# Performance work log

Measured on AMD Instinct MI355X. Metric: run time of the kernel, lower is better.

The kernel has to match this reference:

```python
import jax, jax.numpy as jnp
import numpy as np

B, T, N, F, H, HEADS = 4, 10, 2048, 64, 128, 4
D = H // HEADS
E = 65536
NTOT = B * N


def setup_inputs() -> dict:
    key = jax.random.key(0)
    ks = jax.random.split(key, 16)
    s = 0.05
    return {
        "x": jax.random.normal(ks[0], (B, T, N, F), jnp.float32),
        "W": jax.random.normal(ks[1], (F, H), jnp.float32) * s,
        "att_src": jax.random.normal(ks[2], (HEADS, D), jnp.float32) * s,
        "att_dst": jax.random.normal(ks[3], (HEADS, D), jnp.float32) * s,
        "gat_bias": jnp.zeros((H,), jnp.float32),
        "W_ih0": jax.random.normal(ks[4], (4 * H, H), jnp.float32) * s,
        "W_hh0": jax.random.normal(ks[5], (4 * H, H), jnp.float32) * s,
        "b_ih0": jnp.zeros((4 * H,), jnp.float32),
        "b_hh0": jnp.zeros((4 * H,), jnp.float32),
        "W_ih1": jax.random.normal(ks[6], (4 * H, H), jnp.float32) * s,
        "W_hh1": jax.random.normal(ks[7], (4 * H, H), jnp.float32) * s,
        "b_ih1": jnp.zeros((4 * H,), jnp.float32),
        "b_hh1": jnp.zeros((4 * H,), jnp.float32),
        "ln_gamma": jnp.ones((H,), jnp.float32),
        "ln_beta": jnp.zeros((H,), jnp.float32),
        "edge_index": jax.random.randint(ks[8], (2, E), 0, NTOT, dtype=jnp.int32),
    }


def reference(x, W, att_src, att_dst, gat_bias,
              W_ih0, W_hh0, b_ih0, b_hh0,
              W_ih1, W_hh1, b_ih1, b_hh1,
              ln_gamma, ln_beta, edge_index):
    # ---- GAT spatial encoding, vectorized over all T timesteps ----
    loops = jnp.arange(NTOT, dtype=edge_index.dtype)  # PyG GATConv adds self-loops
    src = jnp.concatenate([edge_index[0], loops])
    dst = jnp.concatenate([edge_index[1], loops])

    x_flat = x.transpose(1, 0, 2, 3).reshape(T, NTOT, F)          # [T, B*N, F]
    h = (x_flat @ W).reshape(T, NTOT, HEADS, D)                    # per-head projections
    a_src = jnp.einsum('tnhd,hd->tnh', h, att_src)                 # [T, NTOT, HEADS]
    a_dst = jnp.einsum('tnhd,hd->tnh', h, att_dst)
    e = jax.nn.leaky_relu(a_src[:, src] + a_dst[:, dst], 0.2)      # [T, Ef, HEADS]

    def seg_softmax(e_t):
        m = jax.ops.segment_max(e_t, dst, num_segments=NTOT)
        ex = jnp.exp(e_t - m[dst])
        den = jax.ops.segment_sum(ex, dst, num_segments=NTOT)
        return ex / den[dst]

    alpha = jax.vmap(seg_softmax)(e)                               # edge softmax per target
    msg = alpha[..., None] * h[:, src]                             # [T, Ef, HEADS, D]
    agg = jax.vmap(lambda m: jax.ops.segment_sum(m, dst, num_segments=NTOT))(msg)
    spatial = jax.nn.relu(agg.reshape(T, NTOT, H) + gat_bias)      # concat heads + bias + relu

    # ---- 2-layer LSTM over time (batched over all B*N node sequences) ----
    def step(carry, xt):
        h0, c0, h1, c1 = carry
        g0 = xt @ W_ih0.T + h0 @ W_hh0.T + (b_ih0 + b_hh0)
        i, f, g, o = jnp.split(g0, 4, axis=-1)
        c0 = jax.nn.sigmoid(f) * c0 + jax.nn.sigmoid(i) * jnp.tanh(g)
        h0 = jax.nn.sigmoid(o) * jnp.tanh(c0)
        g1 = h0 @ W_ih1.T + h1 @ W_hh1.T + (b_ih1 + b_hh1)
        i, f, g, o = jnp.split(g1, 4, axis=-1)
        c1 = jax.nn.sigmoid(f) * c1 + jax.nn.sigmoid(i) * jnp.tanh(g)
        h1 = jax.nn.sigmoid(o) * jnp.tanh(c1)
        return (h0, c0, h1, c1), None

    z = jnp.zeros((NTOT, H), spatial.dtype)
    (_, _, h1, _), _ = jax.lax.scan(step, (z, z, z, z), spatial)
    ctx = h1.reshape(B, N, H)

    # ---- LayerNorm ----
    mu = ctx.mean(-1, keepdims=True)
    var = ctx.var(-1, keepdims=True)
    return (ctx - mu) / jnp.sqrt(var + 1e-5) * ln_gamma + ln_beta
```

## Files before the change

### kernel.cpp

```cpp
#include <hip/hip_runtime.h>

#define T_ 10
#define B_ 4
#define N_ 2048
#define NTOT 8192
#define F_ 64
#define H_ 128
#define NHEADS 4
#define D_ 32
#define E_ 65536
#define EF 73728
#define HPAD 136

typedef __bf16 bf16x8 __attribute__((ext_vector_type(8)));
typedef float f32x4 __attribute__((ext_vector_type(4)));
typedef unsigned short u16;

__device__ __forceinline__ float bf2f(u16 u){
  union { unsigned int i; float f; } v; v.i = ((unsigned int)u) << 16; return v.f;
}
__device__ __forceinline__ u16 f2bf(float f){
  union { float f; unsigned int i; } v; v.f = f;
  return (u16)((v.i + 0x7FFFu + ((v.i >> 16) & 1u)) >> 16);
}
__device__ __forceinline__ float rcpf(float x){ return __builtin_amdgcn_rcpf(x); }
__device__ __forceinline__ float sigf(float x){ return rcpf(1.f + __expf(-x)); }
__device__ __forceinline__ float tanhfast(float x){ return 1.f - 2.f * rcpf(__expf(2.f * x) + 1.f); }
__device__ __forceinline__ float lrelu(float x){ return x > 0.f ? x : 0.2f * x; }

__global__ __launch_bounds__(256) void k_init(int* __restrict__ cnt){
  int i = blockIdx.x * 256 + threadIdx.x;
  if(i < NTOT) cnt[i] = 0;
}

__global__ __launch_bounds__(256) void k_count(const int* __restrict__ ei, int* __restrict__ cnt){
  int e = blockIdx.x * 256 + threadIdx.x;
  if(e < E_) atomicAdd(&cnt[ei[E_ + e]], 1);
}

__global__ __launch_bounds__(1024) void k_scan(const int* __restrict__ cnt,
                                               int* __restrict__ rowst,
                                               int* __restrict__ cursor){
  __shared__ int lds[1024];
  const int t = threadIdx.x;
  int loc[8];
  int s = 0;
  #pragma unroll
  for(int i = 0; i < 8; i++){ loc[i] = s; s += cnt[t * 8 + i]; }
  lds[t] = s;
  __syncthreads();
  for(int off = 1; off < 1024; off <<= 1){
    int v = lds[t];
    int a = (t >= off) ? lds[t - off] : 0;
    __syncthreads();
    lds[t] = v + a;
    __syncthreads();
  }
  const int base = (t > 0) ? lds[t - 1] : 0;
  #pragma unroll
  for(int i = 0; i < 8; i++){
    rowst[t * 8 + i] = base + loc[i];
    cursor[t * 8 + i] = 0;
  }
  if(t == 1023) rowst[NTOT] = lds[1023];
}

__global__ __launch_bounds__(256) void k_fill(const int* __restrict__ ei,
                                              const int* __restrict__ rowst,
                                              int* __restrict__ cursor,
                                              int* __restrict__ csr,
                                              int* __restrict__ csr_dst){
  int e = blockIdx.x * 256 + threadIdx.x;
  if(e < E_){
    int d = ei[E_ + e];
    int pos = atomicAdd(&cursor[d], 1);
    csr[rowst[d] + pos] = ei[e];
    csr_dst[rowst[d] + pos] = d;
  }
}

__global__ __launch_bounds__(256) void k_wconv(const float* __restrict__ s0, u16* __restrict__ d0,
                                               const float* __restrict__ s1, u16* __restrict__ d1,
                                               const float* __restrict__ s2, u16* __restrict__ d2,
                                               const float* __restrict__ s3, u16* __restrict__ d3,
                                               const float* __restrict__ W, u16* __restrict__ Wt){
  int i = blockIdx.x * 256 + threadIdx.x;
  if(blockIdx.y == 4){
    if(i < H_ * F_){
      int nn = i >> 6, f = i & 63;
      Wt[i] = f2bf(W[f * H_ + nn]);
    }
    return;
  }
  const float* src = blockIdx.y == 0 ? s0 : blockIdx.y == 1 ? s1 : blockIdx.y == 2 ? s2 : s3;
  u16* dst = blockIdx.y == 0 ? d0 : blockIdx.y == 1 ? d1 : blockIdx.y == 2 ? d2 : d3;
  if(i < 512 * 128){
    int p = i >> 7, k = i & 127;
    int w = p >> 6, g = (p >> 4) & 3, l = p & 15;
    int row = g * 128 + w * 16 + l;
    dst[i] = f2bf(src[row * 128 + k]);
  }
}

__global__ __launch_bounds__(256) void k_projm(const float* __restrict__ x,
    const u16* __restrict__ Wt, const float* __restrict__ att_s, const float* __restrict__ att_d,
    u16* __restrict__ hbuf, float* __restrict__ asrc, float* __restrict__ adst){
  const int tid  = threadIdx.x;
  const int wave = tid >> 6;
  const int lane = tid & 63;
  const int l15  = lane & 15;
  const int quad = lane >> 4;
  const int r0   = blockIdx.x * 64 + wave * 16;
  const int row  = r0 + l15;
  const int t = row >> 13, nt = row & 8191;
  const int b = nt >> 11, n = nt & 2047;
  const float* xrow = x + (((size_t)b * T_ + t) * N_ + n) * F_;

  bf16x8 a[2];
  #pragma unroll
  for(int ks = 0; ks < 2; ks++){
    const float4 f0 = *(const float4*)(xrow + ks * 32 + quad * 8);
    const float4 f1 = *(const float4*)(xrow + ks * 32 + quad * 8 + 4);
    bf16x8 av;
    av[0] = (__bf16)f0.x; av[1] = (__bf16)f0.y; av[2] = (__bf16)f0.z; av[3] = (__bf16)f0.w;
    av[4] = (__bf16)f1.x; av[5] = (__bf16)f1.y; av[6] = (__bf16)f1.z; av[7] = (__bf16)f1.w;
    a[ks] = av;
  }

  f32x4 acc[8];
  #pragma unroll
  for(int c = 0; c < 8; c++){ f32x4 z = {0.f,0.f,0.f,0.f}; acc[c] = z; }
  #pragma unroll
  for(int c = 0; c < 8; c++){
    #pragma unroll
    for(int ks = 0; ks < 2; ks++){
      const bf16x8 bv = *(const bf16x8*)(Wt + (c * 16 + l15) * F_ + ks * 32 + quad * 8);
      acc[c] = __builtin_amdgcn_mfma_f32_16x16x32_bf16(a[ks], bv, acc[c], 0, 0, 0);
    }
  }

  float ps[4][4], pd[4][4];
  #pragma unroll
  for(int r = 0; r < 4; r++)
    #pragma unroll
    for(int h = 0; h < 4; h++){ ps[r][h] = 0.f; pd[r][h] = 0.f; }

  #pragma unroll
  for(int c = 0; c < 8; c++){
    const int col = c * 16 + l15;
    const float asv = att_s[col];
    const float adv = att_d[col];
    const int head = c >> 1;
    #pragma unroll
    for(int r = 0; r < 4; r++){
      const float v = acc[c][r];
      hbuf[(size_t)(r0 + quad * 4 + r) * H_ + col] = f2bf(v);
      ps[r][head] += v * asv;
      pd[r][head] += v * adv;
    }
  }
  #pragma unroll
  for(int m = 8; m >= 1; m >>= 1){
    #pragma unroll
    for(int r = 0; r < 4; r++)
      #pragma unroll
      for(int h = 0; h < 4; h++){
        ps[r][h] += __shfl_xor(ps[r][h], m);
        pd[r][h] += __shfl_xor(pd[r][h], m);
      }
  }
  if(l15 == 0){
    #pragma unroll
    for(int r = 0; r < 4; r++){
      const int rw = r0 + quad * 4 + r;
      #pragma unroll
      for(int h = 0; h < 4; h++){
        asrc[(size_t)rw * NHEADS + h] = ps[r][h];
        adst[(size_t)rw * NHEADS + h] = pd[r][h];
      }
    }
  }
}

__global__ __launch_bounds__(256) void k_mden(const float* __restrict__ asrc,
    const float* __restrict__ adst, const int* __restrict__ rowst, const int* __restrict__ csr,
    float* __restrict__ m_, float* __restrict__ den_){
  const int gid = blockIdx.x * 256 + threadIdx.x;
  const int head = gid & 3;
  const int node = (gid >> 2) & 8191;
  const int t = gid >> 15;
  const int rbase = t * NTOT;
  const float ad = adst[(size_t)(rbase + node) * NHEADS + head];
  float m = lrelu(asrc[(size_t)(rbase + node) * NHEADS + head] + ad);
  float den = 1.f;
  const int rs = rowst[node], re = rowst[node + 1];
  for(int i = rs; i < re; i++){
    const int s = csr[i];
    const float ev = lrelu(asrc[(size_t)(rbase + s) * NHEADS + head] + ad);
    const float nm = fmaxf(m, ev);
    den = den * __expf(m - nm) + __expf(ev - nm);
    m = nm;
  }
  m_[gid] = m;
  den_[gid] = den;
}

__global__ __launch_bounds__(256) void k_alpha(const float* __restrict__ asrc,
    const float* __restrict__ adst, const int* __restrict__ csr, const int* __restrict__ csr_dst,
    const float* __restrict__ m_, const float* __restrict__ den_, float* __restrict__ alphaC){
  const int p = blockIdx.x * 256 + threadIdx.x;
  const int t = blockIdx.y;
  const int rbase = t * NTOT;
  int s, d;
  if(p < E_){ s = csr[p]; d = csr_dst[p]; } else { s = d = p - E_; }
  const float4 as4 = *(const float4*)&asrc[(size_t)(rbase + s) * NHEADS];
  const float4 ad4 = *(const float4*)&adst[(size_t)(rbase + d) * NHEADS];
  const float4 m4  = *(const float4*)&m_[(size_t)(rbase + d) * NHEADS];
  const float4 dn4 = *(const float4*)&den_[(size_t)(rbase + d) * NHEADS];
  float4 o;
  o.x = __expf(lrelu(as4.x + ad4.x) - m4.x) * rcpf(dn4.x);
  o.y = __expf(lrelu(as4.y + ad4.y) - m4.y) * rcpf(dn4.y);
  o.z = __expf(lrelu(as4.z + ad4.z) - m4.z) * rcpf(dn4.z);
  o.w = __expf(lrelu(as4.w + ad4.w) - m4.w) * rcpf(dn4.w);
  *(float4*)&alphaC[((size_t)t * EF + p) * NHEADS] = o;
}

__global__ __launch_bounds__(256) void k_agg(const u16* __restrict__ hbuf,
    const float* __restrict__ alphaC, const int* __restrict__ rowst, const int* __restrict__ csr,
    const float* __restrict__ gbias, u16* __restrict__ spat){
  const int tid = threadIdx.x;
  const int wave = tid >> 6;
  const int lane = tid & 63;
  const int task = blockIdx.x * 4 + wave;
  const int node = task & 8191;
  const int t = task >> 13;
  const int rbase = t * NTOT;
  const int d0 = lane, d1 = lane + 64;

  const float4 aself = *(const float4*)&alphaC[((size_t)t * EF + E_ + node) * NHEADS];
  float acc0 = (lane < 32 ? aself.x : aself.y) * bf2f(hbuf[(size_t)(rbase + node) * H_ + d0]);
  float acc1 = (lane < 32 ? aself.z : aself.w) * bf2f(hbuf[(size_t)(rbase + node) * H_ + d1]);
  const int rs = rowst[node], re = rowst[node + 1];
  for(int i = rs; i < re; i++){
    const int s = csr[i];
    const float4 av = *(const float4*)&alphaC[((size_t)t * EF + i) * NHEADS];
    const float a0 = lane < 32 ? av.x : av.y;
    const float a1 = lane < 32 ? av.z : av.w;
    acc0 += a0 * bf2f(hbuf[(size_t)(rbase + s) * H_ + d0]);
    acc1 += a1 * bf2f(hbuf[(size_t)(rbase + s) * H_ + d1]);
  }
  const float v0 = acc0 + gbias[d0];
  const float v1 = acc1 + gbias[d1];
  spat[(size_t)(rbase + node) * H_ + d0] = f2bf(v0 > 0.f ? v0 : 0.f);
  spat[(size_t)(rbase + node) * H_ + d1] = f2bf(v1 > 0.f ? v1 : 0.f);
}

__global__ __launch_bounds__(512) void k_lstm(
    const u16* __restrict__ spat,
    const u16* __restrict__ Wp_ih0, const u16* __restrict__ Wp_hh0,
    const float* __restrict__ bih0, const float* __restrict__ bhh0,
    const u16* __restrict__ Wp_ih1, const u16* __restrict__ Wp_hh1,
    const float* __restrict__ bih1, const float* __restrict__ bhh1,
    const float* __restrict__ lng, const float* __restrict__ lnb,
    float* __restrict__ out)
{
  __shared__ __align__(16) u16 xin[32 * HPAD];
  __shared__ __align__(16) u16 h0s[2][32 * HPAD];
  __shared__ __align__(16) u16 h1s[2][32 * HPAD];
  __shared__ __align__(16) float hfin[32 * 129];
  __shared__ float cst_l[16][512];
  __shared__ float bias_l[8][512];

  const int tid  = threadIdx.x;
  const int wave = tid >> 6;
  const int lane = tid & 63;
  const int l15  = lane & 15;
  const int quad = lane >> 4;
  const int n0   = blockIdx.x * 32;
  const int dim  = wave * 16 + l15;

  for(int i = tid; i < 2 * 32 * HPAD; i += 512){
    ((u16*)h0s)[i] = 0; ((u16*)h1s)[i] = 0;
  }
  {
    const u16* src = spat + (size_t)n0 * H_;
    const int r = tid >> 4, c = tid & 15;
    *(uint4*)(xin + r * HPAD + c * 8) = *(const uint4*)(src + r * 128 + c * 8);
  }
  #pragma unroll
  for(int i = 0; i < 16; i++) cst_l[i][tid] = 0.f;
  #pragma unroll
  for(int g = 0; g < 4; g++){
    bias_l[g][tid]     = bih0[g * 128 + dim] + bhh0[g * 128 + dim];
    bias_l[4 + g][tid] = bih1[g * 128 + dim] + bhh1[g * 128 + dim];
  }
  __syncthreads();

  const size_t fbase = (size_t)(wave * 64 + l15) * 128 + quad * 8;

#define LOADB(BK, MATB, KS, NTO)                                          \
    BK[0] = *(const bf16x8*)((MATB) + (NTO) * 2048 + (KS) * 32);          \
    BK[1] = *(const bf16x8*)((MATB) + ((NTO) + 1) * 2048 + (KS) * 32);

#define LOADA(AP, KS)                                                     \
    a0 = *(const bf16x8*)((AP) + l15 * HPAD + (KS) * 32 + quad * 8);      \
    a1 = *(const bf16x8*)((AP) + (16 + l15) * HPAD + (KS) * 32 + quad * 8);

#define MM(BK, NTO)                                                                             \
    acc[0][NTO]       = __builtin_amdgcn_mfma_f32_16x16x32_bf16(a0, BK[0], acc[0][NTO], 0, 0, 0);       \
    acc[1][NTO]       = __builtin_amdgcn_mfma_f32_16x16x32_bf16(a1, BK[0], acc[1][NTO], 0, 0, 0);       \
    acc[0][(NTO) + 1] = __builtin_amdgcn_mfma_f32_16x16x32_bf16(a0, BK[1], acc[0][(NTO) + 1], 0, 0, 0); \
    acc[1][(NTO) + 1] = __builtin_amdgcn_mfma_f32_16x16x32_bf16(a1, BK[1], acc[1][(NTO) + 1], 0, 0, 0); \
    __builtin_amdgcn_sched_barrier(0);

  #pragma unroll 1
  for(int t = 0; t < T_; t++){
    const int rp = t & 1, wp = rp ^ 1;
    #pragma unroll
    for(int layer = 0; layer < 2; layer++){
      const u16* Wih = layer ? Wp_ih1 : Wp_ih0;
      const u16* Whh = layer ? Wp_hh1 : Wp_hh0;
      const u16* xp  = layer ? h0s[wp] : xin;
      const u16* hp  = layer ? h1s[rp] : h0s[rp];

      f32x4 acc[2][4];
      #pragma unroll
      for(int nt = 0; nt < 4; nt++){
        const float bv = bias_l[layer * 4 + nt][tid];
        f32x4 b4 = {bv, bv, bv, bv};
        acc[0][nt] = b4; acc[1][nt] = b4;
      }

      const u16* WihB = Wih + fbase;
      const u16* WhhB = Whh + fbase;
      bf16x8 bA[2], bB[2], bC[2];
      bf16x8 a0, a1;

      LOADB(bA, WihB, 0, 0)  LOADB(bB, WihB, 0, 2)  LOADA(xp, 0)
      LOADB(bC, WihB, 1, 0)  MM(bA, 0)
      LOADB(bA, WihB, 1, 2)  MM(bB, 2)
      LOADA(xp, 1)  LOADB(bB, WihB, 2, 0)  MM(bC, 0)
      LOADB(bC, WihB, 2, 2)  MM(bA, 2)
      LOADA(xp, 2)  LOADB(bA, WihB, 3, 0)  MM(bB, 0)
      LOADB(bB, WihB, 3, 2)  MM(bC, 2)
      LOADA(xp, 3)  LOADB(bC, WhhB, 0, 0)  MM(bA, 0)
      LOADB(bA, WhhB, 0, 2)  MM(bB, 2)
      LOADA(hp, 0)  LOADB(bB, WhhB, 1, 0)  MM(bC, 0)
      LOADB(bC, WhhB, 1, 2)  MM(bA, 2)
      LOADA(hp, 1)  LOADB(bA, WhhB, 2, 0)  MM(bB, 0)
      LOADB(bB, WhhB, 2, 2)  MM(bC, 2)
      LOADA(hp, 2)  LOADB(bC, WhhB, 3, 0)  MM(bA, 0)
      LOADB(bA, WhhB, 3, 2)  MM(bB, 2)
      LOADA(hp, 3)  MM(bC, 0)
      MM(bA, 2)

      u16* hcur = layer ? h1s[wp] : h0s[wp];
      #pragma unroll
      for(int mt = 0; mt < 2; mt++){
        #pragma unroll
        for(int r = 0; r < 4; r++){
          const int node = mt * 16 + quad * 4 + r;
          const float gi = acc[mt][0][r];
          const float gf = acc[mt][1][r];
          const float gg = acc[mt][2][r];
          const float go = acc[mt][3][r];
          const int ci = layer * 8 + mt * 4 + r;
          const float c = sigf(gf) * cst_l[ci][tid] + sigf(gi) * tanhfast(gg);
          cst_l[ci][tid] = c;
          const float hv = sigf(go) * tanhfast(c);
          hcur[node * HPAD + dim] = f2bf(hv);
          if(layer == 1 && t == T_ - 1)
            hfin[node * 129 + dim] = hv;
        }
      }
      if(layer == 1 && t < T_ - 1){
        const u16* src = spat + (size_t)((t + 1) * NTOT + n0) * H_;
        const int r = tid >> 4, c = tid & 15;
        *(uint4*)(xin + r * HPAD + c * 8) = *(const uint4*)(src + r * 128 + c * 8);
      }
      __syncthreads();
    }
  }
#undef MM
#undef LOADA
#undef LOADB

  {
    const int node = tid >> 4;
    const int c0 = (tid & 15) * 8;
    float v[8];
    #pragma unroll
    for(int j = 0; j < 8; j++) v[j] = hfin[node * 129 + c0 + j];
    float s = 0.f;
    #pragma unroll
    for(int j = 0; j < 8; j++) s += v[j];
    #pragma unroll
    for(int m = 8; m >= 1; m >>= 1) s += __shfl_xor(s, m);
    const float mu = s * (1.f / H_);
    float q = 0.f;
    #pragma unroll
    for(int j = 0; j < 8; j++){ const float d = v[j] - mu; q += d * d; }
    #pragma unroll
    for(int m = 8; m >= 1; m >>= 1) q += __shfl_xor(q, m);
    const float rstd = rsqrtf(q * (1.f / H_) + 1e-5f);
    #pragma unroll
    for(int j = 0; j < 8; j++)
      out[(size_t)(n0 + node) * H_ + c0 + j] = (v[j] - mu) * rstd * lng[c0 + j] + lnb[c0 + j];
  }
}

extern "C" void kernel_launch(void* const* d_in, const int* in_sizes, int n_in,
                              void* d_out, int out_size, void* d_ws, size_t ws_size,
                              hipStream_t stream) {
  (void)in_sizes; (void)n_in; (void)out_size; (void)ws_size;
  const float* x     = (const float*)d_in[0];
  const float* W     = (const float*)d_in[1];
  const float* att_s = (const float*)d_in[2];
  const float* att_d = (const float*)d_in[3];
  const float* gbias = (const float*)d_in[4];
  const float* Wih0  = (const float*)d_in[5];
  const float* Whh0  = (const float*)d_in[6];
  const float* bih0  = (const float*)d_in[7];
  const float* bhh0  = (const float*)d_in[8];
  const float* Wih1  = (const float*)d_in[9];
  const float* Whh1  = (const float*)d_in[10];
  const float* bih1  = (const float*)d_in[11];
  const float* bhh1  = (const float*)d_in[12];
  const float* lng   = (const float*)d_in[13];
  const float* lnb   = (const float*)d_in[14];
  const int*   ei    = (const int*)d_in[15];
  float* out = (float*)d_out;

  char* p = (char*)d_ws;
  auto carve = [&](size_t bytes) -> void* {
    void* r = (void*)p;
    p += (bytes + 255) & ~(size_t)255;
    return r;
  };
  u16* Wp_ih0 = (u16*)carve(512 * 128 * 2);
  u16* Wp_hh0 = (u16*)carve(512 * 128 * 2);
  u16* Wp_ih1 = (u16*)carve(512 * 128 * 2);
  u16* Wp_hh1 = (u16*)carve(512 * 128 * 2);
  u16* Wt     = (u16*)carve(H_ * F_ * 2);
  u16*   hbuf   = (u16*)carve((size_t)T_ * NTOT * H_ * 2);
  float* asrc   = (float*)carve((size_t)T_ * NTOT * NHEADS * 4);
  float* adst   = (float*)carve((size_t)T_ * NTOT * NHEADS * 4);
  float* m_     = (float*)carve((size_t)T_ * NTOT * NHEADS * 4);
  float* den_   = (float*)carve((size_t)T_ * NTOT * NHEADS * 4);
  float* alphaC = (float*)carve((size_t)T_ * EF * NHEADS * 4);
  u16*   spat   = (u16*)carve((size_t)T_ * NTOT * H_ * 2);
  int*   cnt    = (int*)carve(NTOT * 4);
  int*   curs   = (int*)carve(NTOT * 4);
  int*   rowst  = (int*)carve((NTOT + 1) * 4);
  int*   csr    = (int*)carve((size_t)E_ * 4);
  int*   csrd   = (int*)carve((size_t)E_ * 4);

  hipLaunchKernelGGL(k_init,  dim3(32),        dim3(256),  0, stream, cnt);
  hipLaunchKernelGGL(k_count, dim3(256),       dim3(256),  0, stream, ei, cnt);
  hipLaunchKernelGGL(k_scan,  dim3(1),         dim3(1024), 0, stream, cnt, rowst, curs);
  hipLaunchKernelGGL(k_fill,  dim3(256),       dim3(256),  0, stream, ei, rowst, curs, csr, csrd);
  hipLaunchKernelGGL(k_wconv, dim3(256, 5),    dim3(256),  0, stream,
                     Wih0, Wp_ih0, Whh0, Wp_hh0, Wih1, Wp_ih1, Whh1, Wp_hh1, W, Wt);
  hipLaunchKernelGGL(k_projm, dim3(1280),      dim3(256),  0, stream, x, Wt, att_s, att_d, hbuf, asrc, adst);
  hipLaunchKernelGGL(k_mden,  dim3(1280),      dim3(256),  0, stream, asrc, adst, rowst, csr, m_, den_);
  hipLaunchKernelGGL(k_alpha, dim3(288, 10),   dim3(256),  0, stream, asrc, adst, csr, csrd, m_, den_, alphaC);
  hipLaunchKernelGGL(k_agg,   dim3(20480),     dim3(256),  0, stream, hbuf, alphaC, rowst, csr, gbias, spat);
  hipLaunchKernelGGL(k_lstm,  dim3(256),       dim3(512),  0, stream, spat,
                     Wp_ih0, Wp_hh0, bih0, bhh0, Wp_ih1, Wp_hh1, bih1, bhh1, lng, lnb, out);
}
```

Measured before the change: 338.3 us.

## Fuse GAT softmax max/denominator, alpha, and aggregation into one kernel

Replaces the separate k_mden, k_alpha and k_agg kernels with a single per-node wave kernel. Each wave computes the online softmax max and denominator over its incoming edges with a lane-parallel pass and a shuffle reduction, then recomputes the edge weights on the fly while aggregating neighbour features. This removes two launches and the global round trips through the m, den and alpha buffers. In exchange, every lane recomputes exp and leaky-relu for each edge in the aggregation loop.

```diff
diff --git a/kernel.cpp b/kernel.cpp
--- a/kernel.cpp
+++ b/kernel.cpp
@@ -182,51 +182,9 @@
   }
 }
 
-__global__ __launch_bounds__(256) void k_mden(const float* __restrict__ asrc,
-    const float* __restrict__ adst, const int* __restrict__ rowst, const int* __restrict__ csr,
-    float* __restrict__ m_, float* __restrict__ den_){
-  const int gid = blockIdx.x * 256 + threadIdx.x;
-  const int head = gid & 3;
-  const int node = (gid >> 2) & 8191;
-  const int t = gid >> 15;
-  const int rbase = t * NTOT;
-  const float ad = adst[(size_t)(rbase + node) * NHEADS + head];
-  float m = lrelu(asrc[(size_t)(rbase + node) * NHEADS + head] + ad);
-  float den = 1.f;
-  const int rs = rowst[node], re = rowst[node + 1];
-  for(int i = rs; i < re; i++){
-    const int s = csr[i];
-    const float ev = lrelu(asrc[(size_t)(rbase + s) * NHEADS + head] + ad);
-    const float nm = fmaxf(m, ev);
-    den = den * __expf(m - nm) + __expf(ev - nm);
-    m = nm;
-  }
-  m_[gid] = m;
-  den_[gid] = den;
-}
-
-__global__ __launch_bounds__(256) void k_alpha(const float* __restrict__ asrc,
-    const float* __restrict__ adst, const int* __restrict__ csr, const int* __restrict__ csr_dst,
-    const float* __restrict__ m_, const float* __restrict__ den_, float* __restrict__ alphaC){
-  const int p = blockIdx.x * 256 + threadIdx.x;
-  const int t = blockIdx.y;
-  const int rbase = t * NTOT;
-  int s, d;
-  if(p < E_){ s = csr[p]; d = csr_dst[p]; } else { s = d = p - E_; }
-  const float4 as4 = *(const float4*)&asrc[(size_t)(rbase + s) * NHEADS];
-  const float4 ad4 = *(const float4*)&adst[(size_t)(rbase + d) * NHEADS];
-  const float4 m4  = *(const float4*)&m_[(size_t)(rbase + d) * NHEADS];
-  const float4 dn4 = *(const float4*)&den_[(size_t)(rbase + d) * NHEADS];
-  float4 o;
-  o.x = __expf(lrelu(as4.x + ad4.x) - m4.x) * rcpf(dn4.x);
-  o.y = __expf(lrelu(as4.y + ad4.y) - m4.y) * rcpf(dn4.y);
-  o.z = __expf(lrelu(as4.z + ad4.z) - m4.z) * rcpf(dn4.z);
-  o.w = __expf(lrelu(as4.w + ad4.w) - m4.w) * rcpf(dn4.w);
-  *(float4*)&alphaC[((size_t)t * EF + p) * NHEADS] = o;
-}
-
-__global__ __launch_bounds__(256) void k_agg(const u16* __restrict__ hbuf,
-    const float* __restrict__ alphaC, const int* __restrict__ rowst, const int* __restrict__ csr,
+__global__ __launch_bounds__(256) void k_gat(const u16* __restrict__ hbuf,
+    const float* __restrict__ asrc, const float* __restrict__ adst,
+    const int* __restrict__ rowst, const int* __restrict__ csr,
     const float* __restrict__ gbias, u16* __restrict__ spat){
   const int tid = threadIdx.x;
   const int wave = tid >> 6;
@@ -235,24 +193,62 @@
   const int node = task & 8191;
   const int t = task >> 13;
   const int rbase = t * NTOT;
-  const int d0 = lane, d1 = lane + 64;
-
-  const float4 aself = *(const float4*)&alphaC[((size_t)t * EF + E_ + node) * NHEADS];
-  float acc0 = (lane < 32 ? aself.x : aself.y) * bf2f(hbuf[(size_t)(rbase + node) * H_ + d0]);
-  float acc1 = (lane < 32 ? aself.z : aself.w) * bf2f(hbuf[(size_t)(rbase + node) * H_ + d1]);
   const int rs = rowst[node], re = rowst[node + 1];
+
+  const float4 ad4  = *(const float4*)&adst[(size_t)(rbase + node) * NHEADS];
+  const float4 ass4 = *(const float4*)&asrc[(size_t)(rbase + node) * NHEADS];
+  const float es0 = lrelu(ass4.x + ad4.x), es1 = lrelu(ass4.y + ad4.y);
+  const float es2 = lrelu(ass4.z + ad4.z), es3 = lrelu(ass4.w + ad4.w);
+
+  float m0, m1, m2, m3, d0, d1, d2, d3;
+  if(lane == 0){ m0 = es0; m1 = es1; m2 = es2; m3 = es3; d0 = d1 = d2 = d3 = 1.f; }
+  else { m0 = m1 = m2 = m3 = -1e30f; d0 = d1 = d2 = d3 = 0.f; }
+  for(int i = rs + lane; i < re; i += 64){
+    const int s = csr[i];
+    const float4 as4 = *(const float4*)&asrc[(size_t)(rbase + s) * NHEADS];
+    const float e0 = lrelu(as4.x + ad4.x), e1 = lrelu(as4.y + ad4.y);
+    const float e2 = lrelu(as4.z + ad4.z), e3 = lrelu(as4.w + ad4.w);
+    float nm;
+    nm = fmaxf(m0, e0); d0 = d0 * __expf(m0 - nm) + __expf(e0 - nm); m0 = nm;
+    nm = fmaxf(m1, e1); d1 = d1 * __expf(m1 - nm) + __expf(e1 - nm); m1 = nm;
+    nm = fmaxf(m2, e2); d2 = d2 * __expf(m2 - nm) + __expf(e2 - nm); m2 = nm;
+    nm = fmaxf(m3, e3); d3 = d3 * __expf(m3 - nm) + __expf(e3 - nm); m3 = nm;
+  }
+  #pragma unroll
+  for(int msk = 32; msk >= 1; msk >>= 1){
+    float mo, dn, nm;
+    mo = __shfl_xor(m0, msk); dn = __shfl_xor(d0, msk);
+    nm = fmaxf(m0, mo); d0 = d0 * __expf(m0 - nm) + dn * __expf(mo - nm); m0 = nm;
+    mo = __shfl_xor(m1, msk); dn = __shfl_xor(d1, msk);
+    nm = fmaxf(m1, mo); d1 = d1 * __expf(m1 - nm) + dn * __expf(mo - nm); m1 = nm;
+    mo = __shfl_xor(m2, msk); dn = __shfl_xor(d2, msk);
+    nm = fmaxf(m2, mo); d2 = d2 * __expf(m2 - nm) + dn * __expf(mo - nm); m2 = nm;
+    mo = __shfl_xor(m3, msk); dn = __shfl_xor(d3, msk);
+    nm = fmaxf(m3, mo); d3 = d3 * __expf(m3 - nm) + dn * __expf(mo - nm); m3 = nm;
+  }
+
+  const int dlo = lane, dhi = lane + 64;
+  const float mA  = lane < 32 ? m0 : m1;
+  const float mB  = lane < 32 ? m2 : m3;
+  const float rdA = rcpf(lane < 32 ? d0 : d1);
+  const float rdB = rcpf(lane < 32 ? d2 : d3);
+  const float esA = lane < 32 ? es0 : es1;
+  const float esB = lane < 32 ? es2 : es3;
+
+  float acc0 = __expf(esA - mA) * rdA * bf2f(hbuf[(size_t)(rbase + node) * H_ + dlo]);
+  float acc1 = __expf(esB - mB) * rdB * bf2f(hbuf[(size_t)(rbase + node) * H_ + dhi]);
   for(int i = rs; i < re; i++){
     const int s = csr[i];
-    const float4 av = *(const float4*)&alphaC[((size_t)t * EF + i) * NHEADS];
-    const float a0 = lane < 32 ? av.x : av.y;
-    const float a1 = lane < 32 ? av.z : av.w;
-    acc0 += a0 * bf2f(hbuf[(size_t)(rbase + s) * H_ + d0]);
-    acc1 += a1 * bf2f(hbuf[(size_t)(rbase + s) * H_ + d1]);
-  }
-  const float v0 = acc0 + gbias[d0];
-  const float v1 = acc1 + gbias[d1];
-  spat[(size_t)(rbase + node) * H_ + d0] = f2bf(v0 > 0.f ? v0 : 0.f);
-  spat[(size_t)(rbase + node) * H_ + d1] = f2bf(v1 > 0.f ? v1 : 0.f);
+    const float4 as4 = *(const float4*)&asrc[(size_t)(rbase + s) * NHEADS];
+    const float eA = lane < 32 ? lrelu(as4.x + ad4.x) : lrelu(as4.y + ad4.y);
+    const float eB = lane < 32 ? lrelu(as4.z + ad4.z) : lrelu(as4.w + ad4.w);
+    acc0 += __expf(eA - mA) * rdA * bf2f(hbuf[(size_t)(rbase + s) * H_ + dlo]);
+    acc1 += __expf(eB - mB) * rdB * bf2f(hbuf[(size_t)(rbase + s) * H_ + dhi]);
+  }
+  const float v0 = acc0 + gbias[dlo];
+  const float v1 = acc1 + gbias[dhi];
+  spat[(size_t)(rbase + node) * H_ + dlo] = f2bf(v0 > 0.f ? v0 : 0.f);
+  spat[(size_t)(rbase + node) * H_ + dhi] = f2bf(v1 > 0.f ? v1 : 0.f);
 }
 
 __global__ __launch_bounds__(512) void k_lstm(
@@ -445,9 +441,6 @@
   u16*   hbuf   = (u16*)carve((size_t)T_ * NTOT * H_ * 2);
   float* asrc   = (float*)carve((size_t)T_ * NTOT * NHEADS * 4);
   float* adst   = (float*)carve((size_t)T_ * NTOT * NHEADS * 4);
-  float* m_     = (float*)carve((size_t)T_ * NTOT * NHEADS * 4);
-  float* den_   = (float*)carve((size_t)T_ * NTOT * NHEADS * 4);
-  float* alphaC = (float*)carve((size_t)T_ * EF * NHEADS * 4);
   u16*   spat   = (u16*)carve((size_t)T_ * NTOT * H_ * 2);
   int*   cnt    = (int*)carve(NTOT * 4);
   int*   curs   = (int*)carve(NTOT * 4);
@@ -462,9 +455,7 @@
   hipLaunchKernelGGL(k_wconv, dim3(256, 5),    dim3(256),  0, stream,
                      Wih0, Wp_ih0, Whh0, Wp_hh0, Wih1, Wp_ih1, Whh1, Wp_hh1, W, Wt);
   hipLaunchKernelGGL(k_projm, dim3(1280),      dim3(256),  0, stream, x, Wt, att_s, att_d, hbuf, asrc, adst);
-  hipLaunchKernelGGL(k_mden,  dim3(1280),      dim3(256),  0, stream, asrc, adst, rowst, csr, m_, den_);
-  hipLaunchKernelGGL(k_alpha, dim3(288, 10),   dim3(256),  0, stream, asrc, adst, csr, csrd, m_, den_, alphaC);
-  hipLaunchKernelGGL(k_agg,   dim3(20480),     dim3(256),  0, stream, hbuf, alphaC, rowst, csr, gbias, spat);
+  hipLaunchKernelGGL(k_gat,   dim3(20480),     dim3(256),  0, stream, hbuf, asrc, adst, rowst, csr, gbias, spat);
   hipLaunchKernelGGL(k_lstm,  dim3(256),       dim3(512),  0, stream, spat,
                      Wp_ih0, Wp_hh0, bih0, bhh0, Wp_ih1, Wp_hh1, bih1, bhh1, lng, lnb, out);
 }
```

After: 388.3 us. 1.15x slower.
